# Performance work log

Hardware: AMD Instinct MI355X
Metric: run time of the kernel (lower is better)

The kernel has to match this reference:

```python
import jax, jax.numpy as jnp
import numpy as np

B, S, K, N, G = 4, 2048, 4096, 11008, 128  # batch, seq, in_features, out_features, groupsize


def setup_inputs() -> dict:
    key = jax.random.key(0)
    k1, k2, k3, k4 = jax.random.split(key, 4)
    x = jax.random.normal(k1, (B, S, K), dtype=jnp.float32)
    # unpacked int4 codes in [0, 16)
    weight_q = jax.random.randint(k2, (N, K), 0, 16, dtype=jnp.int32)
    # groupwise scales (positive, small) and zeros, packed as [K//G, N, 2]
    scales = jax.random.uniform(k3, (K // G, N), dtype=jnp.float32) * 0.02 + 1e-3
    zeros = jax.random.normal(k4, (K // G, N), dtype=jnp.float32) * 0.1
    scales_and_zeros = jnp.stack([scales, zeros], axis=-1)  # [K//G, N, 2]
    return {"x": x, "weight_q": weight_q, "scales_and_zeros": scales_and_zeros}


def reference(x, weight_q, scales_and_zeros):
    # Dequantize groupwise: w[n,k] = (q[n,k] - 8) * scale[k//G, n] + zero[k//G, n]
    scales = scales_and_zeros[..., 0].T  # [N, K//G]
    zeros = scales_and_zeros[..., 1].T   # [N, K//G]
    q = weight_q.astype(x.dtype).reshape(N, K // G, G)  # [N, K//G, G]
    w = (q - 8.0) * scales[:, :, None] + zeros[:, :, None]  # fused dequant
    w = w.reshape(N, K)
    # y[b,s,n] = sum_k x[b,s,k] * w[n,k]
    return jnp.einsum("bsk,nk->bsn", x, w)
```

## Files before the change

kernel.cpp:

```cpp
#include <hip/hip_runtime.h>
#include <stdint.h>


typedef __attribute__((ext_vector_type(8))) short short8;
typedef __attribute__((ext_vector_type(4))) float float4v;
typedef __attribute__((ext_vector_type(4))) int int4v;
typedef __attribute__((ext_vector_type(2))) float float2v;
typedef __attribute__((ext_vector_type(4))) unsigned short ushort4v;

static constexpr int M_ = 8192;
static constexpr int K_ = 4096;
static constexpr int N_ = 11008;

__device__ __forceinline__ unsigned short f2bf(float f) {
    union { float f; uint32_t u; } v;
    v.f = f;
    uint32_t u = v.u;
    u += 0x7fffu + ((u >> 16) & 1u);
    return (unsigned short)(u >> 16);
}

__device__ __forceinline__ void gload16(const void* g, void* l) {
    __builtin_amdgcn_global_load_lds(
        (const __attribute__((address_space(1))) uint32_t*)g,
        (__attribute__((address_space(3))) uint32_t*)l, 16, 0, 0);
}

__global__ __launch_bounds__(256) void cvt_x_kernel(const float* __restrict__ X,
                                                    unsigned short* __restrict__ Xb) {
    const int i = blockIdx.x * 256 + threadIdx.x;
    const float4v a = ((const float4v*)X)[2 * (size_t)i];
    const float4v b = ((const float4v*)X)[2 * (size_t)i + 1];
    short8 o;
    #pragma unroll
    for (int j = 0; j < 4; ++j) o[j] = (short)f2bf(a[j]);
    #pragma unroll
    for (int j = 0; j < 4; ++j) o[4 + j] = (short)f2bf(b[j]);
    ((short8*)Xb)[(size_t)i] = o;
}

__global__ __launch_bounds__(256) void deq_w_kernel(const int* __restrict__ Q,
                                                    const float* __restrict__ SZ,
                                                    unsigned short* __restrict__ Wb) {
    const int i = blockIdx.x * 256 + threadIdx.x;
    const int n = i >> 9;
    const int c = i & 511;
    const int k0 = c * 8;
    const int g = k0 >> 7;
    const float2v sz = *(const float2v*)(SZ + ((size_t)g * N_ + n) * 2);
    const float s = sz[0], z = sz[1];
    const int4v q0 = *(const int4v*)(Q + (size_t)n * K_ + k0);
    const int4v q1 = *(const int4v*)(Q + (size_t)n * K_ + k0 + 4);
    short8 o;
    #pragma unroll
    for (int j = 0; j < 4; ++j) o[j] = (short)f2bf((float)(q0[j] - 8) * s + z);
    #pragma unroll
    for (int j = 0; j < 4; ++j) o[4 + j] = (short)f2bf((float)(q1[j] - 8) * s + z);
    ((short8*)Wb)[(size_t)i] = o;
}


#define SBAR() __builtin_amdgcn_sched_barrier(0)
#define VMW0() asm volatile("s_waitcnt vmcnt(0)" ::: "memory")
#define LGKM0() asm volatile("s_waitcnt lgkmcnt(0)" ::: "memory")
#define BARRIER() __builtin_amdgcn_s_barrier()

__global__ __launch_bounds__(512, 4) void gemm_bf16_2cu(
    const unsigned short* __restrict__ Agl,
    const unsigned short* __restrict__ Bgl,
    float* __restrict__ C) {
    __shared__ alignas(16) unsigned short lds[24576];

    const int tid = threadIdx.x;
    const int lane = tid & 63;
    const int wid = tid >> 6;
    const int wr = wid >> 1;
    const int wc = wid & 1;

    const int bid = blockIdx.x;
    const int wg = (bid & 7) * 344 + (bid >> 3);
    const int mt = wg / 86;
    const int nt = wg % 86;
    const int row0 = mt * 256;
    const int col0 = nt * 128;

    const int srow = lane >> 2;
    const int kc = ((lane & 3) ^ ((lane >> 3) & 3)) * 8;

    const int l15 = lane & 15;
    const int lg = lane >> 4;
    const int pslot = (lg ^ ((l15 >> 1) & 3)) << 4;
    const int aB = (wr * 64 + l15) * 64 + pslot;
    const int bB = 32768 + (wc * 64 + l15) * 64 + pslot;

    const char* ldsB = (const char*)lds;
    unsigned short* ldsU = lds;
    const char* AglB = (const char*)Agl;
    const char* BglB = (const char*)Bgl;

    uint32_t sa0 = (uint32_t)(row0 + wid * 32 + 0 + srow) * (K_ * 2) + (uint32_t)kc * 2;
    uint32_t sa1 = (uint32_t)(row0 + wid * 32 + 16 + srow) * (K_ * 2) + (uint32_t)kc * 2;
    uint32_t sb0 = (uint32_t)(col0 + wid * 16 + srow) * (K_ * 2) + (uint32_t)kc * 2;

    auto stage = [&](int b) {
        gload16(AglB + sa0, ldsU + b * 8192 + (wid * 32 + 0) * 32);          sa0 += 64;
        gload16(AglB + sa1, ldsU + b * 8192 + (wid * 32 + 16) * 32);         sa1 += 64;
        gload16(BglB + sb0, ldsU + 16384 + b * 4096 + (wid * 16) * 32);      sb0 += 64;
    };

    float4v acc[4][4] = {};

    stage(0);
    VMW0();
    BARRIER(); SBAR();

#define KTILE(BUF, DN)                                                        \
    {                                                                         \
        if (DN) stage((BUF) ^ 1);                                             \
        short8 af[4], bf[4];                                                  \
        _Pragma("unroll")                                                     \
        for (int mf = 0; mf < 4; ++mf)                                        \
            af[mf] = *(const short8*)(ldsB + (BUF) * 16384 + mf * 1024 + aB); \
        _Pragma("unroll")                                                     \
        for (int nf = 0; nf < 4; ++nf)                                        \
            bf[nf] = *(const short8*)(ldsB + (BUF) * 8192 + nf * 1024 + bB);  \
        LGKM0(); SBAR();                                                      \
        __builtin_amdgcn_s_setprio(1);                                        \
        _Pragma("unroll")                                                     \
        for (int mf = 0; mf < 4; ++mf)                                        \
            _Pragma("unroll")                                                 \
            for (int nf = 0; nf < 4; ++nf)                                    \
                acc[mf][nf] = __builtin_amdgcn_mfma_f32_16x16x32_bf16(        \
                    af[mf], bf[nf], acc[mf][nf], 0, 0, 0);                    \
        __builtin_amdgcn_s_setprio(0);                                        \
        if (DN) {                                                             \
            VMW0();                                                           \
            BARRIER(); SBAR();                                                \
        }                                                                     \
    }

    for (int t2 = 0; t2 < 126; t2 += 2) {
        KTILE(0, 1);
        KTILE(1, 1);
    }
    KTILE(0, 1);
    KTILE(1, 0);
#undef KTILE

    const int lrow = lg * 4;
    #pragma unroll
    for (int mf = 0; mf < 4; ++mf)
        #pragma unroll
        for (int nf = 0; nf < 4; ++nf)
            #pragma unroll
            for (int j = 0; j < 4; ++j) {
                const int r = row0 + wr * 64 + mf * 16 + lrow + j;
                const int c = col0 + wc * 64 + nf * 16 + l15;
                C[(size_t)r * N_ + c] = acc[mf][nf][j];
            }
}

static constexpr int LDSS = 40;

__global__ __launch_bounds__(256, 2) void w4_gemm_fused(
    const float* __restrict__ X, const int* __restrict__ Q,
    const float* __restrict__ SZ, float* __restrict__ C) {
    __shared__ alignas(16) unsigned short As[128 * LDSS];
    __shared__ alignas(16) unsigned short Ws[128 * LDSS];
    const int tid = threadIdx.x;
    const int lane = tid & 63;
    const int wid = tid >> 6;
    const int wrr = wid >> 1;
    const int wcc = wid & 1;
    const int row0 = blockIdx.x * 128;
    const int col0 = blockIdx.y * 128;
    float4v acc[4][4] = {};
    float4v a_reg[4];
    int4v q_reg[4];
    float2v sz_reg[4];

    auto load_tile = [&](int kb) {
        const int g = kb >> 7;
        #pragma unroll
        for (int i = 0; i < 4; ++i) {
            const int idx = tid + 256 * i;
            const int r = idx >> 3;
            const int v = idx & 7;
            a_reg[i] = *(const float4v*)(X + (size_t)(row0 + r) * K_ + kb + v * 4);
            q_reg[i] = *(const int4v*)(Q + (size_t)(col0 + r) * K_ + kb + v * 4);
            sz_reg[i] = *(const float2v*)(SZ + ((size_t)g * N_ + (col0 + r)) * 2);
        }
    };
    auto write_tile = [&]() {
        #pragma unroll
        for (int i = 0; i < 4; ++i) {
            const int idx = tid + 256 * i;
            const int r = idx >> 3;
            const int v = idx & 7;
            ushort4v ab, wb;
            #pragma unroll
            for (int j = 0; j < 4; ++j) ab[j] = f2bf(a_reg[i][j]);
            const float s = sz_reg[i][0];
            const float z = sz_reg[i][1];
            #pragma unroll
            for (int j = 0; j < 4; ++j) wb[j] = f2bf((float)(q_reg[i][j] - 8) * s + z);
            *(ushort4v*)(&As[r * LDSS + v * 4]) = ab;
            *(ushort4v*)(&Ws[r * LDSS + v * 4]) = wb;
        }
    };
    auto compute = [&]() {
        const int lr = lane & 15;
        const int lgg = lane >> 4;
        short8 af[4], bf[4];
        #pragma unroll
        for (int mf = 0; mf < 4; ++mf)
            af[mf] = *(const short8*)(&As[(wrr * 64 + mf * 16 + lr) * LDSS + lgg * 8]);
        #pragma unroll
        for (int nf = 0; nf < 4; ++nf)
            bf[nf] = *(const short8*)(&Ws[(wcc * 64 + nf * 16 + lr) * LDSS + lgg * 8]);
        #pragma unroll
        for (int mf = 0; mf < 4; ++mf)
            #pragma unroll
            for (int nf = 0; nf < 4; ++nf)
                acc[mf][nf] = __builtin_amdgcn_mfma_f32_16x16x32_bf16(
                    af[mf], bf[nf], acc[mf][nf], 0, 0, 0);
    };

    load_tile(0);
    for (int kb = 0; kb < K_; kb += 32) {
        __syncthreads();
        write_tile();
        __syncthreads();
        if (kb + 32 < K_) load_tile(kb + 32);
        compute();
    }
    const int lr = lane & 15;
    const int lgg = lane >> 4;
    #pragma unroll
    for (int mf = 0; mf < 4; ++mf)
        #pragma unroll
        for (int nf = 0; nf < 4; ++nf)
            #pragma unroll
            for (int j = 0; j < 4; ++j) {
                const int r = row0 + wrr * 64 + mf * 16 + lgg * 4 + j;
                const int c = col0 + wcc * 64 + nf * 16 + lr;
                C[(size_t)r * N_ + c] = acc[mf][nf][j];
            }
}

extern "C" void kernel_launch(void* const* d_in, const int* in_sizes, int n_in,
                              void* d_out, int out_size, void* d_ws, size_t ws_size,
                              hipStream_t stream) {
    const float* X  = (const float*)d_in[0];
    const int*   Q  = (const int*)d_in[1];
    const float* SZ = (const float*)d_in[2];
    float* C = (float*)d_out;

    const size_t xb_bytes = (size_t)M_ * K_ * 2;
    const size_t wb_bytes = (size_t)N_ * K_ * 2;
    if (ws_size >= xb_bytes + wb_bytes) {
        unsigned short* Xb = (unsigned short*)d_ws;
        unsigned short* Wb = (unsigned short*)((char*)d_ws + xb_bytes);
        cvt_x_kernel<<<(M_ * (K_ / 8)) / 256, 256, 0, stream>>>(X, Xb);
        deq_w_kernel<<<(N_ * (K_ / 8)) / 256, 256, 0, stream>>>(Q, SZ, Wb);
        gemm_bf16_2cu<<<dim3(2752), dim3(512), 0, stream>>>(Xb, Wb, C);
    } else {
        dim3 grid(M_ / 128, N_ / 128);
        w4_gemm_fused<<<grid, dim3(256), 0, stream>>>(X, Q, SZ, C);
    }
}
```

Before: 867.1 us.

## Pre-swizzle weights into MFMA fragment order and load B directly to registers

The dequant kernel now writes bf16 weights in a layout that matches the MFMA B-fragment order (16 rows by 32 k per 64-lane block). The GEMM then loads B fragments straight from global memory into registers, skipping the LDS staging. A is staged through a deeper 4-buffer LDS ring with partial vmcnt waits instead of full drains. This reduces LDS traffic and synchronisation for B, at the cost of more in-flight global loads per thread and more LDS for A.

```diff
diff --git a/kernel.cpp b/kernel.cpp
--- a/kernel.cpp
+++ b/kernel.cpp
@@ -43,10 +43,13 @@
                                                     const float* __restrict__ SZ,
                                                     unsigned short* __restrict__ Wb) {
     const int i = blockIdx.x * 256 + threadIdx.x;
-    const int n = i >> 9;
-    const int c = i & 511;
-    const int k0 = c * 8;
-    const int g = k0 >> 7;
+    const int lane = i & 63;
+    const int rest = i >> 6;
+    const int kb = rest & 127;
+    const int nb = rest >> 7;
+    const int n = nb * 16 + (lane & 15);
+    const int k0 = kb * 32 + (lane >> 4) * 8;
+    const int g = kb >> 2;
     const float2v sz = *(const float2v*)(SZ + ((size_t)g * N_ + n) * 2);
     const float s = sz[0], z = sz[1];
     const int4v q0 = *(const int4v*)(Q + (size_t)n * K_ + k0);
@@ -61,15 +64,15 @@
 
 
 #define SBAR() __builtin_amdgcn_sched_barrier(0)
-#define VMW0() asm volatile("s_waitcnt vmcnt(0)" ::: "memory")
+#define VMW(n) asm volatile("s_waitcnt vmcnt(" #n ")" ::: "memory")
 #define LGKM0() asm volatile("s_waitcnt lgkmcnt(0)" ::: "memory")
 #define BARRIER() __builtin_amdgcn_s_barrier()
 
-__global__ __launch_bounds__(512, 4) void gemm_bf16_2cu(
+__global__ __launch_bounds__(512, 4) void gemm_bf16_hyb(
     const unsigned short* __restrict__ Agl,
-    const unsigned short* __restrict__ Bgl,
+    const unsigned short* __restrict__ Wt,
     float* __restrict__ C) {
-    __shared__ alignas(16) unsigned short lds[24576];
+    __shared__ alignas(16) unsigned short lds[32768];
 
     const int tid = threadIdx.x;
     const int lane = tid & 63;
@@ -91,40 +94,50 @@
     const int lg = lane >> 4;
     const int pslot = (lg ^ ((l15 >> 1) & 3)) << 4;
     const int aB = (wr * 64 + l15) * 64 + pslot;
-    const int bB = 32768 + (wc * 64 + l15) * 64 + pslot;
 
     const char* ldsB = (const char*)lds;
     unsigned short* ldsU = lds;
     const char* AglB = (const char*)Agl;
-    const char* BglB = (const char*)Bgl;
+    const char* WtB = (const char*)Wt;
 
     uint32_t sa0 = (uint32_t)(row0 + wid * 32 + 0 + srow) * (K_ * 2) + (uint32_t)kc * 2;
     uint32_t sa1 = (uint32_t)(row0 + wid * 32 + 16 + srow) * (K_ * 2) + (uint32_t)kc * 2;
-    uint32_t sb0 = (uint32_t)(col0 + wid * 16 + srow) * (K_ * 2) + (uint32_t)kc * 2;
+
+#define BOFF(nf) \
+    (uint32_t)(((uint32_t)(nt * 8 + wc * 4 + (nf)) * 128 * 64 + lane) * 16)
+    uint32_t bo0 = BOFF(0), bo1 = BOFF(1), bo2 = BOFF(2), bo3 = BOFF(3);
+#undef BOFF
+
+    float4v acc[4][4] = {};
+    short8 af[4], bf[4];
 
     auto stage = [&](int b) {
-        gload16(AglB + sa0, ldsU + b * 8192 + (wid * 32 + 0) * 32);          sa0 += 64;
-        gload16(AglB + sa1, ldsU + b * 8192 + (wid * 32 + 16) * 32);         sa1 += 64;
-        gload16(BglB + sb0, ldsU + 16384 + b * 4096 + (wid * 16) * 32);      sb0 += 64;
-    };
-
-    float4v acc[4][4] = {};
-
-    stage(0);
-    VMW0();
+        gload16(AglB + sa0, ldsU + b * 8192 + (wid * 32 + 0) * 32);  sa0 += 64;
+        gload16(AglB + sa1, ldsU + b * 8192 + (wid * 32 + 16) * 32); sa1 += 64;
+    };
+    auto loadB = [&]() {
+        bf[0] = *(const short8*)(WtB + bo0); bo0 += 1024;
+        bf[1] = *(const short8*)(WtB + bo1); bo1 += 1024;
+        bf[2] = *(const short8*)(WtB + bo2); bo2 += 1024;
+        bf[3] = *(const short8*)(WtB + bo3); bo3 += 1024;
+    };
+
+    stage(0); stage(1);
+    SBAR();
+    loadB();
+    SBAR();
+    VMW(2);
     BARRIER(); SBAR();
 
-#define KTILE(BUF, DN)                                                        \
+#define KTILE(BUF, DN, W, LB)                                                 \
     {                                                                         \
-        if (DN) stage((BUF) ^ 1);                                             \
-        short8 af[4], bf[4];                                                  \
+        if (DN) stage(((BUF) + 2) & 3);                                       \
+        SBAR();                                                               \
         _Pragma("unroll")                                                     \
         for (int mf = 0; mf < 4; ++mf)                                        \
             af[mf] = *(const short8*)(ldsB + (BUF) * 16384 + mf * 1024 + aB); \
-        _Pragma("unroll")                                                     \
-        for (int nf = 0; nf < 4; ++nf)                                        \
-            bf[nf] = *(const short8*)(ldsB + (BUF) * 8192 + nf * 1024 + bB);  \
         LGKM0(); SBAR();                                                      \
+        VMW(W); SBAR();                                                       \
         __builtin_amdgcn_s_setprio(1);                                        \
         _Pragma("unroll")                                                     \
         for (int mf = 0; mf < 4; ++mf)                                        \
@@ -133,18 +146,22 @@
                 acc[mf][nf] = __builtin_amdgcn_mfma_f32_16x16x32_bf16(        \
                     af[mf], bf[nf], acc[mf][nf], 0, 0, 0);                    \
         __builtin_amdgcn_s_setprio(0);                                        \
-        if (DN) {                                                             \
-            VMW0();                                                           \
-            BARRIER(); SBAR();                                                \
-        }                                                                     \
-    }
-
-    for (int t2 = 0; t2 < 126; t2 += 2) {
-        KTILE(0, 1);
-        KTILE(1, 1);
-    }
-    KTILE(0, 1);
-    KTILE(1, 0);
+        SBAR();                                                               \
+        if (LB) loadB();                                                      \
+        SBAR();                                                               \
+        BARRIER(); SBAR();                                                    \
+    }
+
+    for (int t2 = 0; t2 < 124; t2 += 4) {
+        KTILE(0, 1, 2, 1);
+        KTILE(1, 1, 2, 1);
+        KTILE(2, 1, 2, 1);
+        KTILE(3, 1, 2, 1);
+    }
+    KTILE(0, 1, 2, 1);
+    KTILE(1, 1, 2, 1);
+    KTILE(2, 0, 0, 1);
+    KTILE(3, 0, 0, 0);
 #undef KTILE
 
     const int lrow = lg * 4;
@@ -263,7 +280,7 @@
         unsigned short* Wb = (unsigned short*)((char*)d_ws + xb_bytes);
         cvt_x_kernel<<<(M_ * (K_ / 8)) / 256, 256, 0, stream>>>(X, Xb);
         deq_w_kernel<<<(N_ * (K_ / 8)) / 256, 256, 0, stream>>>(Q, SZ, Wb);
-        gemm_bf16_2cu<<<dim3(2752), dim3(512), 0, stream>>>(Xb, Wb, C);
+        gemm_bf16_hyb<<<dim3(2752), dim3(512), 0, stream>>>(Xb, Wb, C);
     } else {
         dim3 grid(M_ / 128, N_ / 128);
         w4_gemm_fused<<<grid, dim3(256), 0, stream>>>(X, Q, SZ, C);
```

Result: slower. 1.097 ms (+26.6%).
